# Optimization experiments

Measured on AMD Instinct MI355X. Metric: run time of the kernel, lower is better.

The kernel has to match this reference:

```python
import math
import jax, jax.numpy as jnp
from jax import lax
import numpy as np

B, DIM, H, W = 8, 256, 64, 64
D_STATE, D_CONV, EXPAND = 16, 4, 2
D_INNER = EXPAND * DIM
DT_RANK = math.ceil(DIM / 16)
POS_LEN = 16
EPS = 1e-5
GN_GROUPS = 32


def setup_inputs() -> dict:
    key = jax.random.key(0)
    ks = iter(jax.random.split(key, 24))
    rn = lambda shape, s=0.02: jax.random.normal(next(ks), shape, jnp.float32) * s
    inp = {}
    inp["x"] = jax.random.normal(next(ks), (B, DIM, H, W), jnp.float32)
    inp["pos_emb"] = rn((1, DIM, POS_LEN), 1.0)
    inp["ln_g"] = jnp.ones((DIM,), jnp.float32)
    inp["ln_b"] = jnp.zeros((DIM,), jnp.float32)
    inp["m_in_w"] = rn((2, 2 * D_INNER, DIM))
    inp["m_conv_w"] = rn((2, D_INNER, D_CONV), 0.1)
    inp["m_conv_b"] = jnp.zeros((2, D_INNER), jnp.float32)
    inp["m_xproj_w"] = rn((2, DT_RANK + 2 * D_STATE, D_INNER))
    inp["m_dt_w"] = rn((2, D_INNER, DT_RANK), 0.1)
    inp["m_dt_b"] = rn((2, D_INNER), 0.1)
    inp["m_A_log"] = jnp.tile(jnp.log(jnp.arange(1, D_STATE + 1, dtype=jnp.float32))[None, None, :], (2, D_INNER, 1))
    inp["m_D"] = jnp.ones((2, D_INNER), jnp.float32)
    inp["m_out_w"] = rn((2, DIM, D_INNER))
    inp["proj_w"] = rn((DIM, 2 * DIM))
    inp["proj_b"] = jnp.zeros((DIM,), jnp.float32)
    inp["up_dw_w"] = rn((DIM, 1, 3, 3), 0.1)
    inp["up_bn1_g"] = jnp.ones((DIM,), jnp.float32)
    inp["up_bn1_b"] = jnp.zeros((DIM,), jnp.float32)
    inp["up_pw_w"] = rn((DIM, DIM), 0.05)
    inp["up_bn2_g"] = jnp.ones((DIM,), jnp.float32)
    inp["up_bn2_b"] = jnp.zeros((DIM,), jnp.float32)
    inp["down_pw_w"] = rn((DIM, DIM), 0.05)
    inp["down_bn_g"] = jnp.ones((DIM,), jnp.float32)
    inp["down_bn_b"] = jnp.zeros((DIM,), jnp.float32)
    inp["gn_g"] = jnp.ones((DIM,), jnp.float32)
    inp["gn_b"] = jnp.zeros((DIM,), jnp.float32)
    return inp


def reference(x, pos_emb, ln_g, ln_b, m_in_w, m_conv_w, m_conv_b, m_xproj_w, m_dt_w, m_dt_b,
              m_A_log, m_D, m_out_w, proj_w, proj_b, up_dw_w, up_bn1_g, up_bn1_b, up_pw_w,
              up_bn2_g, up_bn2_b, down_pw_w, down_bn_g, down_bn_b, gn_g, gn_b):
    Bx, C, Hh, Ww = x.shape

    def ln(t):  # LayerNorm over last dim (shared self.norm)
        m = jnp.mean(t, -1, keepdims=True)
        v = jnp.mean((t - m) ** 2, -1, keepdims=True)
        return (t - m) * lax.rsqrt(v + EPS) * ln_g + ln_b

    def bn(t, g, b):  # BatchNorm2d in eval mode with default running stats (mean 0, var 1)
        return t * (g / jnp.sqrt(1.0 + EPS))[None, :, None, None] + b[None, :, None, None]

    def gn(t):  # GroupNorm(32, C), shared params (self.bn)
        Bn, Cn, Hn, Wn = t.shape
        tg = t.reshape(Bn, GN_GROUPS, Cn // GN_GROUPS, Hn, Wn)
        m = jnp.mean(tg, (2, 3, 4), keepdims=True)
        v = jnp.mean((tg - m) ** 2, (2, 3, 4), keepdims=True)
        tg = (tg - m) * lax.rsqrt(v + EPS)
        return tg.reshape(Bn, Cn, Hn, Wn) * gn_g[None, :, None, None] + gn_b[None, :, None, None]

    def interp_pos(N):  # F.interpolate(pos_embed, size=N, mode='linear', align_corners=False)
        coords = jnp.maximum((jnp.arange(N, dtype=jnp.float32) + 0.5) * (POS_LEN / N) - 0.5, 0.0)
        i0 = jnp.floor(coords).astype(jnp.int32)
        i1 = jnp.minimum(i0 + 1, POS_LEN - 1)
        wgt = coords - i0.astype(jnp.float32)
        return pos_emb[:, :, i0] * (1.0 - wgt) + pos_emb[:, :, i1] * wgt  # (1,C,N)

    def pe_branch(vals, idx, N):  # vals (B,C,N); indices interp at same size = identity
        t = vals + interp_pos(N) + idx.astype(jnp.float32)
        return ln(jnp.swapaxes(t, 1, 2))  # (B,N,C)

    def mamba(u, d):  # standard mamba_ssm selective scan; u (B,L,C)
        xz = jnp.einsum('blc,ic->bli', u, m_in_w[d])
        xh, zg = jnp.split(xz, 2, -1)
        xc = lax.conv_general_dilated(jnp.swapaxes(xh, 1, 2), m_conv_w[d][:, None, :], (1,),
                                      [(D_CONV - 1, 0)], feature_group_count=D_INNER,
                                      dimension_numbers=('NCH', 'OIH', 'NCH'))
        xc = jnp.swapaxes(jax.nn.silu(xc + m_conv_b[d][None, :, None]), 1, 2)  # (B,L,di)
        dbl = jnp.einsum('bld,ed->ble', xc, m_xproj_w[d])
        dt = dbl[..., :DT_RANK]
        Bm = dbl[..., DT_RANK:DT_RANK + D_STATE]
        Cm = dbl[..., DT_RANK + D_STATE:]
        dt = jax.nn.softplus(jnp.einsum('blr,dr->bld', dt, m_dt_w[d]) + m_dt_b[d])  # (B,L,di)
        A = -jnp.exp(m_A_log[d])  # (di,ds)
        dA = jnp.exp(dt[..., None] * A)  # (B,L,di,ds)
        dBx = dt[..., None] * Bm[:, :, None, :] * xc[..., None]

        def step(h, inps):
            dA_t, dBx_t, C_t = inps
            h = dA_t * h + dBx_t
            return h, jnp.einsum('bds,bs->bd', h, C_t)

        h0 = jnp.zeros((u.shape[0], D_INNER, D_STATE), u.dtype)
        _, ys = lax.scan(step, h0, (jnp.swapaxes(dA, 0, 1), jnp.swapaxes(dBx, 0, 1), jnp.swapaxes(Cm, 0, 1)))
        y = jnp.swapaxes(ys, 0, 1) + xc * m_D[d]
        y = y * jax.nn.silu(zg)
        return jnp.einsum('bld,od->blo', y, m_out_w[d])

    # z branch: depthwise ConvTranspose2d(k3,s2,p1,op1) + BN + ReLU + pw conv + BN, then ReLU6
    z = lax.conv_general_dilated(x, jnp.flip(up_dw_w, (2, 3)), (1, 1), [(1, 2), (1, 2)],
                                 lhs_dilation=(2, 2), feature_group_count=C,
                                 dimension_numbers=('NCHW', 'OIHW', 'NCHW'))  # (B,C,2H,2W)
    z = jax.nn.relu(bn(z, up_bn1_g, up_bn1_b))
    z = jnp.einsum('bchw,oc->bohw', z, up_pw_w)
    z = jnp.clip(bn(z, up_bn2_g, up_bn2_b), 0.0, 6.0)

    col_max = pe_branch(jnp.max(x, 2), jnp.argmax(x, 2), Ww)
    col_min = pe_branch(jnp.min(x, 2), jnp.argmin(x, 2), Ww)
    row_max = pe_branch(jnp.max(x, 3), jnp.argmax(x, 3), Hh)
    row_min = pe_branch(jnp.min(x, 3), jnp.argmin(x, 3), Hh)
    result_max = jnp.concatenate([col_max, row_max], 1)  # (B, W+H, C)
    result_min = jnp.concatenate([col_min, row_min], 1)

    fm_max = ln(mamba(result_max, 0))
    fm_min = ln(mamba(result_min, 0))
    bm_max = ln(mamba(jnp.flip(result_max, 1), 1))
    bm_min = ln(mamba(jnp.flip(result_min, 1), 1))

    res_max = jnp.concatenate([fm_max, jnp.flip(bm_max, 1)], -1) @ proj_w.T + proj_b
    res_min = jnp.concatenate([fm_min, jnp.flip(bm_min, 1)], -1) @ proj_w.T + proj_b
    res_max = ln(res_max)[:, :, None, :]  # (B,L,1,C)
    res_min = ln(res_min)[:, None, :, :]  # (B,1,L,C)

    res = jnp.transpose(res_max + res_min, (0, 3, 1, 2))  # (B,C,L,L), L=H+W=2H
    res = jnp.clip(res + 3.0, 0.0, 6.0) / 6.0 * z  # h_sigmoid gate
    res = gn(res)
    res = jnp.einsum('bchw,oc->bohw', res[:, :, ::2, ::2], down_pw_w)  # pw conv stride 2
    res = bn(res, down_bn_g, down_bn_b)
    res = gn(res)
    res = res + x
    res = gn(res)
    return res
```

## Files before the change

### kernel.cpp

```cpp
#include <hip/hip_runtime.h>
#include <hip/hip_bf16.h>
#include <math.h>

typedef __hip_bfloat16 bf16;
typedef __attribute__((ext_vector_type(8))) short short8_t;
typedef __attribute__((ext_vector_type(4))) short short4_t;
typedef __attribute__((ext_vector_type(4))) float f32x4_t;

#define EPSV 1e-5f
#define BNSC 0.99999500003749968f

__device__ __forceinline__ float bf2f(bf16 v){ return __bfloat162float(v); }
__device__ __forceinline__ bf16 f2bf(float v){ return __float2bfloat16(v); }

__device__ __forceinline__ float blk_sum(float v, float* sm){
  int tid = threadIdx.x;
  #pragma unroll
  for(int o=32;o>0;o>>=1) v += __shfl_down(v, o, 64);
  if((tid&63)==0) sm[tid>>6] = v;
  __syncthreads();
  float s = 0.f;
  int nw = blockDim.x>>6;
  for(int i=0;i<nw;i++) s += sm[i];
  __syncthreads();
  return s;
}

__device__ __forceinline__ float softplusf(float x){
  return (x > 20.f) ? x : __logf(1.f + __expf(x));
}
__device__ __forceinline__ float siluf(float x){
  return x / (1.f + __expf(-x));
}

__global__ void prep_weights(const float* __restrict__ in_w, const float* __restrict__ out_w,
                             const float* __restrict__ pw_w, const float* __restrict__ dpw_w,
                             const float* __restrict__ proj_w, const float* __restrict__ xproj_w,
                             bf16* __restrict__ Winb, bf16* __restrict__ Woutb,
                             bf16* __restrict__ Wub, bf16* __restrict__ Wdb,
                             bf16* __restrict__ Wxpb, float* __restrict__ PT,
                             float* __restrict__ gacc){
  int idx = blockIdx.x*256 + threadIdx.x;
  if(idx < 6656) gacc[idx] = 0.f;
  if(idx < 524288){ Winb[idx] = f2bf(in_w[idx]); return; }
  if(idx < 786432){ int i=idx-524288; Woutb[i] = f2bf(out_w[i]); return; }
  if(idx < 851968){ int i=idx-786432; Wub[i] = f2bf(pw_w[i]); return; }
  if(idx < 917504){ int i=idx-851968; Wdb[i] = f2bf(dpw_w[i]); return; }
  if(idx < 1048576){
    int k = idx - 917504;
    int i = k >> 9, j = k & 511;
    PT[j*256 + i] = proj_w[k];
    return;
  }
  int i = idx - 1048576;
  Wxpb[i] = f2bf(xproj_w[i]);
}

__global__ __launch_bounds__(256)
void r1_reduce_pe(const float* __restrict__ x, const float* __restrict__ pe,
                  float* __restrict__ pmax, float* __restrict__ pmin,
                  float* __restrict__ xs, float* __restrict__ xq){
  __shared__ float tile[64*65];
  __shared__ float rs_[4], rq_[4];
  int bc = blockIdx.x;
  int b = bc >> 8, c = bc & 255;
  const float* xp = x + ((size_t)bc << 12);
  float s = 0.f, q = 0.f;
  for(int i=threadIdx.x; i<4096; i+=256){
    float v = xp[i];
    tile[(i>>6)*65 + (i&63)] = v;
    s += v; q += v*v;
  }
  #pragma unroll
  for(int o=32;o>0;o>>=1){ s += __shfl_down(s, o, 64); q += __shfl_down(q, o, 64); }
  int wv = threadIdx.x >> 6, t = threadIdx.x & 63;
  if(t == 0){ rs_[wv] = s; rq_[wv] = q; }
  __syncthreads();
  if(threadIdx.x == 0){
    xs[bc] = rs_[0]+rs_[1]+rs_[2]+rs_[3];
    xq[bc] = rq_[0]+rq_[1]+rq_[2]+rq_[3];
  }
  if(wv >= 2) return;
  float coords = fmaxf((t + 0.5f)*0.25f - 0.5f, 0.f);
  int i0 = (int)floorf(coords);
  int i1 = min(i0+1, 15);
  float wg = coords - (float)i0;
  float pos = pe[c*16+i0]*(1.f-wg) + pe[c*16+i1]*wg;
  if(wv == 0){
    float cmx=-3.4e38f, cmn=3.4e38f; int cax=0, can=0;
    for(int h=0;h<64;h++){
      float v = tile[h*65 + t];
      if(v > cmx){ cmx=v; cax=h; }
      if(v < cmn){ cmn=v; can=h; }
    }
    size_t base_col = ((size_t)b*128 + t)*256 + c;
    pmax[base_col] = cmx + pos + (float)cax;
    pmin[base_col] = cmn + pos + (float)can;
  } else {
    float rmx=-3.4e38f, rmn=3.4e38f; int rax=0, ran=0;
    for(int w=0;w<64;w++){
      float v = tile[t*65 + w];
      if(v > rmx){ rmx=v; rax=w; }
      if(v < rmn){ rmn=v; ran=w; }
    }
    size_t base_row = ((size_t)b*128 + 64 + t)*256 + c;
    pmax[base_row] = rmx + pos + (float)rax;
    pmin[base_row] = rmn + pos + (float)ran;
  }
}

__global__ void ln_rows2(float* __restrict__ bufA, float* __restrict__ bufB,
                         const float* __restrict__ g, const float* __restrict__ bb,
                         bf16* __restrict__ boutA, bf16* __restrict__ boutB){
  __shared__ float sm[8];
  int row = blockIdx.x, t = threadIdx.x;
  float* buf; bf16* bout;
  if(row < 1024){ buf = bufA; bout = boutA; }
  else { buf = bufB; bout = boutB; row -= 1024; }
  float v = buf[(size_t)row*256 + t];
  float m = blk_sum(v, sm) * (1.f/256.f);
  float dv = v - m;
  float var = blk_sum(dv*dv, sm) * (1.f/256.f);
  float r = dv * rsqrtf(var + EPSV) * g[t] + bb[t];
  buf[(size_t)row*256 + t] = r;
  if(bout) bout[(size_t)row*256 + t] = f2bf(r);
}

__global__ __launch_bounds__(256,2)
void m1_mfma(const bf16* __restrict__ ubmax, const bf16* __restrict__ ubmin,
             const bf16* __restrict__ Win, float* __restrict__ xz){
  __shared__ bf16 att[64*264];
  int bx = blockIdx.x;
  int it = bx & 3, lt = (bx>>2)&1, b = (bx>>3)&7, r = bx>>6;
  int d = r & 1;
  const bf16* u = (r < 2) ? ubmax : ubmin;
  int flip = r & 1;
  int t = threadIdx.x;
  {
    int pr = t>>5, cc = (t&31)*8;
    #pragma unroll
    for(int i=0;i<8;i++){
      int p = pr + i*8;
      int l = lt*64 + p;
      int le = flip ? (127 - l) : l;
      short8_t v = *(const short8_t*)((const short*)u + ((size_t)(b*128 + le))*256 + cc);
      *(short8_t*)&att[p*264 + cc] = v;
    }
  }
  __syncthreads();
  int wv = t>>6, lane = t&63, quad = lane>>4, l16 = lane&15;
  int m0 = wv*64;
  f32x4_t acc[4][4];
  #pragma unroll
  for(int ms=0;ms<4;ms++)
    #pragma unroll
    for(int ns=0;ns<4;ns++) acc[ms][ns] = (f32x4_t){0.f,0.f,0.f,0.f};
  const short* wbase = (const short*)Win + ((size_t)d*1024 + it*256)*256;
  for(int k0=0;k0<256;k0+=32){
    short8_t afr[4], bfr[4];
    #pragma unroll
    for(int ms=0;ms<4;ms++)
      afr[ms] = *(const short8_t*)(wbase + (size_t)(m0 + ms*16 + l16)*256 + k0 + quad*8);
    #pragma unroll
    for(int ns=0;ns<4;ns++)
      bfr[ns] = *(const short8_t*)&att[(ns*16 + l16)*264 + k0 + quad*8];
    #pragma unroll
    for(int ms=0;ms<4;ms++)
      #pragma unroll
      for(int ns=0;ns<4;ns++)
        acc[ms][ns] = __builtin_amdgcn_mfma_f32_16x16x32_bf16(afr[ms], bfr[ns], acc[ms][ns], 0,0,0);
  }
  int rb = r*8 + b;
  #pragma unroll
  for(int ns=0;ns<4;ns++){
    int l = lt*64 + ns*16 + l16;
    float* dst = xz + ((size_t)rb*128 + l)*1024 + it*256;
    #pragma unroll
    for(int ms=0;ms<4;ms++){
      int i = m0 + ms*16 + quad*4;
      *(f32x4_t*)(dst + i) = acc[ms][ns];
    }
  }
}

__global__ __launch_bounds__(256)
void m2_conv(const float* __restrict__ xz, const float* __restrict__ cw,
             const float* __restrict__ cb, float* __restrict__ xc,
             bf16* __restrict__ xcb){
  int i4 = blockIdx.x*256 + threadIdx.x;
  int idx = i4 << 2;
  int row = idx >> 9, dd = idx & 511;
  int gl = row & 127;
  int d = (row >> 10) & 1;
  const float* src = xz + (size_t)row*1024 + dd;
  const float* cwp = cw + (size_t)(d*512 + dd)*4;
  f32x4_t w0 = *(const f32x4_t*)(cwp);
  f32x4_t w1 = *(const f32x4_t*)(cwp+4);
  f32x4_t w2 = *(const f32x4_t*)(cwp+8);
  f32x4_t w3 = *(const f32x4_t*)(cwp+12);
  f32x4_t bias = *(const f32x4_t*)(cb + d*512 + dd);
  f32x4_t z4 = (f32x4_t){0.f,0.f,0.f,0.f};
  f32x4_t t3 = *(const f32x4_t*)(src);
  f32x4_t t2 = (gl>=1) ? *(const f32x4_t*)(src-1024) : z4;
  f32x4_t t1 = (gl>=2) ? *(const f32x4_t*)(src-2048) : z4;
  f32x4_t t0 = (gl>=3) ? *(const f32x4_t*)(src-3072) : z4;
  f32x4_t o;
  o[0] = bias[0] + t0[0]*w0[0] + t1[0]*w0[1] + t2[0]*w0[2] + t3[0]*w0[3];
  o[1] = bias[1] + t0[1]*w1[0] + t1[1]*w1[1] + t2[1]*w1[2] + t3[1]*w1[3];
  o[2] = bias[2] + t0[2]*w2[0] + t1[2]*w2[1] + t2[2]*w2[2] + t3[2]*w2[3];
  o[3] = bias[3] + t0[3]*w3[0] + t1[3]*w3[1] + t2[3]*w3[2] + t3[3]*w3[3];
  alignas(8) bf16 ob[4];
  #pragma unroll
  for(int r=0;r<4;r++){ o[r] = siluf(o[r]); ob[r] = f2bf(o[r]); }
  *(f32x4_t*)(xc + idx) = o;
  *(short4_t*)((short*)xcb + idx) = *(const short4_t*)ob;
}

__global__ __launch_bounds__(256)
void m3_xproj(const bf16* __restrict__ xcb, const bf16* __restrict__ Wxpb,
              float* __restrict__ dbl){
  int r0 = blockIdx.x * 64;
  int d = (r0 >> 10) & 1;
  int t = threadIdx.x;
  int wv = t>>6, lane = t&63, quad = lane>>4, l16 = lane&15;
  int rowl = wv*16 + l16;
  const short* bbase = (const short*)xcb + (size_t)(r0 + rowl)*512;
  const short* abase = (const short*)Wxpb + (size_t)d*48*512;
  f32x4_t acc[3];
  #pragma unroll
  for(int ms=0;ms<3;ms++) acc[ms] = (f32x4_t){0.f,0.f,0.f,0.f};
  #pragma unroll 4
  for(int k0=0;k0<512;k0+=32){
    short8_t bfr = *(const short8_t*)(bbase + k0 + quad*8);
    short8_t afr[3];
    #pragma unroll
    for(int ms=0;ms<3;ms++)
      afr[ms] = *(const short8_t*)(abase + (size_t)(ms*16 + l16)*512 + k0 + quad*8);
    #pragma unroll
    for(int ms=0;ms<3;ms++)
      acc[ms] = __builtin_amdgcn_mfma_f32_16x16x32_bf16(afr[ms], bfr, acc[ms], 0,0,0);
  }
  float* dst = dbl + (size_t)(r0 + rowl)*48;
  #pragma unroll
  for(int ms=0;ms<3;ms++)
    *(f32x4_t*)(dst + ms*16 + quad*4) = acc[ms];
}

__global__ __launch_bounds__(256)
void m4_dt(const float* __restrict__ dbl, const float* __restrict__ dtw,
           const float* __restrict__ dtbias, float* __restrict__ dt){
  int i4 = blockIdx.x*256 + threadIdx.x;
  int idx = i4 << 2;
  int row = idx >> 9, dd = idx & 511;
  int d = (row >> 10) & 1;
  const float* dr = dbl + (size_t)row*48;
  f32x4_t dr0 = *(const f32x4_t*)(dr);
  f32x4_t dr1 = *(const f32x4_t*)(dr+4);
  f32x4_t dr2 = *(const f32x4_t*)(dr+8);
  f32x4_t dr3 = *(const f32x4_t*)(dr+12);
  f32x4_t bias = *(const f32x4_t*)(dtbias + d*512 + dd);
  f32x4_t o;
  #pragma unroll
  for(int j=0;j<4;j++){
    const float* wp = dtw + (size_t)(d*512 + dd + j)*16;
    f32x4_t w0 = *(const f32x4_t*)(wp);
    f32x4_t w1 = *(const f32x4_t*)(wp+4);
    f32x4_t w2 = *(const f32x4_t*)(wp+8);
    f32x4_t w3 = *(const f32x4_t*)(wp+12);
    float s = bias[j];
    s += dr0[0]*w0[0] + dr0[1]*w0[1] + dr0[2]*w0[2] + dr0[3]*w0[3];
    s += dr1[0]*w1[0] + dr1[1]*w1[1] + dr1[2]*w1[2] + dr1[3]*w1[3];
    s += dr2[0]*w2[0] + dr2[1]*w2[1] + dr2[2]*w2[2] + dr2[3]*w2[3];
    s += dr3[0]*w3[0] + dr3[1]*w3[1] + dr3[2]*w3[2] + dr3[3]*w3[3];
    o[j] = softplusf(s);
  }
  *(f32x4_t*)(dt + idx) = o;
}

__global__ void m5_passA(const float* __restrict__ dt, const float* __restrict__ xc,
                         const float* __restrict__ dbl, const float* __restrict__ Alog,
                         float* __restrict__ P, float* __restrict__ Hl){
  int bx = blockIdx.x;
  int seg = bx & 7, half = (bx>>3)&1, rb = bx>>4;
  int dd = half*256 + threadIdx.x;
  int d = (rb>>3)&1;
  float A[16], h[16], pr[16];
  #pragma unroll
  for(int s=0;s<16;s++){
    A[s] = -__expf(Alog[(size_t)(d*512 + dd)*16 + s]);
    h[s] = 0.f; pr[s] = 1.f;
  }
  int l0 = seg*16;
  for(int l=l0;l<l0+16;l++){
    size_t row = (size_t)rb*128 + l;
    float dtv = dt[row*512 + dd];
    float xcv = xc[row*512 + dd];
    float bx_ = dtv*xcv;
    const float* dr = dbl + row*48;
    #pragma unroll
    for(int s=0;s<16;s++){
      float dA = __expf(dtv*A[s]);
      pr[s] *= dA;
      h[s] = dA*h[s] + bx_*dr[16+s];
    }
  }
  size_t o = ((size_t)(rb*8 + seg)*512 + dd)*16;
  #pragma unroll
  for(int s=0;s<16;s+=4){
    *(f32x4_t*)(P  + o + s) = (f32x4_t){pr[s],pr[s+1],pr[s+2],pr[s+3]};
    *(f32x4_t*)(Hl + o + s) = (f32x4_t){h[s],h[s+1],h[s+2],h[s+3]};
  }
}

__global__ void m5_passB(const float* __restrict__ dt, const float* __restrict__ xc,
                         const float* __restrict__ dbl, const float* __restrict__ xz,
                         const float* __restrict__ Alog, const float* __restrict__ Dp,
                         const float* __restrict__ P, const float* __restrict__ Hl,
                         bf16* __restrict__ ybb){
  int bx = blockIdx.x;
  int seg = bx & 7, half = (bx>>3)&1, rb = bx>>4;
  int dd = half*256 + threadIdx.x;
  int d = (rb>>3)&1;
  float A[16], h[16];
  #pragma unroll
  for(int s=0;s<16;s++){
    A[s] = -__expf(Alog[(size_t)(d*512 + dd)*16 + s]);
    h[s] = 0.f;
  }
  for(int j=0;j<seg;j++){
    size_t o = ((size_t)(rb*8 + j)*512 + dd)*16;
    #pragma unroll
    for(int s=0;s<16;s+=4){
      f32x4_t pv = *(const f32x4_t*)(P + o + s);
      f32x4_t hv = *(const f32x4_t*)(Hl + o + s);
      h[s]   = pv[0]*h[s]   + hv[0];
      h[s+1] = pv[1]*h[s+1] + hv[1];
      h[s+2] = pv[2]*h[s+2] + hv[2];
      h[s+3] = pv[3]*h[s+3] + hv[3];
    }
  }
  float Dv = Dp[d*512 + dd];
  int l0 = seg*16;
  for(int l=l0;l<l0+16;l++){
    size_t row = (size_t)rb*128 + l;
    float dtv = dt[row*512 + dd];
    float xcv = xc[row*512 + dd];
    float zgv = xz[row*1024 + 512 + dd];
    const float* dr = dbl + row*48;
    float bx_ = dtv*xcv;
    float y = 0.f;
    #pragma unroll
    for(int s=0;s<16;s++){
      h[s] = __expf(dtv*A[s])*h[s] + bx_*dr[16+s];
      y += h[s]*dr[32+s];
    }
    ybb[row*512 + dd] = f2bf((y + xcv*Dv) * siluf(zgv));
  }
}

__global__ __launch_bounds__(256,2)
void m6_mfma(const bf16* __restrict__ ybb, const bf16* __restrict__ Wout,
             const float* __restrict__ lng, const float* __restrict__ lnb,
             float* __restrict__ mo){
  __shared__ char smem[64*264*4];
  bf16* ybt = (bf16*)smem;
  float* fbuf = (float*)smem;
  int bx = blockIdx.x;
  int lt = bx & 1, b = (bx>>1)&7, r = bx>>4;
  int d = r & 1, rb = r*8 + b;
  size_t rowbase = (size_t)rb*128 + lt*64;
  int t = threadIdx.x;
  for(int i=t;i<4096;i+=256){
    int row = i>>6, c8 = (i&63)*8;
    short8_t v = *(const short8_t*)((const short*)ybb + (rowbase + row)*512 + c8);
    *(short8_t*)&ybt[row*520 + c8] = v;
  }
  __syncthreads();
  int wv = t>>6, lane = t&63, quad = lane>>4, l16 = lane&15;
  int m0 = wv*64;
  f32x4_t acc[4][4];
  #pragma unroll
  for(int ms=0;ms<4;ms++)
    #pragma unroll
    for(int ns=0;ns<4;ns++) acc[ms][ns] = (f32x4_t){0.f,0.f,0.f,0.f};
  const short* wbase = (const short*)Wout + (size_t)d*256*512;
  for(int k0=0;k0<512;k0+=32){
    short8_t afr[4], bfr[4];
    #pragma unroll
    for(int ms=0;ms<4;ms++)
      afr[ms] = *(const short8_t*)(wbase + (size_t)(m0 + ms*16 + l16)*512 + k0 + quad*8);
    #pragma unroll
    for(int ns=0;ns<4;ns++)
      bfr[ns] = *(const short8_t*)&ybt[(ns*16 + l16)*520 + k0 + quad*8];
    #pragma unroll
    for(int ms=0;ms<4;ms++)
      #pragma unroll
      for(int ns=0;ns<4;ns++)
        acc[ms][ns] = __builtin_amdgcn_mfma_f32_16x16x32_bf16(afr[ms], bfr[ns], acc[ms][ns], 0,0,0);
  }
  __syncthreads();
  #pragma unroll
  for(int ns=0;ns<4;ns++){
    int row = ns*16 + l16;
    #pragma unroll
    for(int ms=0;ms<4;ms++){
      int o = m0 + ms*16 + quad*4;
      *(f32x4_t*)(fbuf + row*264 + o) = acc[ms][ns];
    }
  }
  __syncthreads();
  {
    int row = t >> 2, part = t & 3;
    const float* fr = fbuf + row*264;
    float s = 0.f;
    #pragma unroll 8
    for(int j=0;j<64;j++){
      int col = part*64 + ((j + part*16) & 63);
      s += fr[col];
    }
    s += __shfl_xor(s, 1, 64);
    s += __shfl_xor(s, 2, 64);
    float m = s * (1.f/256.f);
    float q = 0.f;
    #pragma unroll 8
    for(int j=0;j<64;j++){
      int col = part*64 + ((j + part*16) & 63);
      float dv = fr[col] - m;
      q += dv*dv;
    }
    q += __shfl_xor(q, 1, 64);
    q += __shfl_xor(q, 2, 64);
    float rs = rsqrtf(q*(1.f/256.f) + EPSV);
    float* dst = mo + (rowbase + row)*256;
    for(int j=0;j<64;j++){
      int col = part*64 + j;
      dst[col] = (fr[col] - m)*rs*lng[col] + lnb[col];
    }
  }
}

__global__ void m7_proj(const float* __restrict__ mo, const float* __restrict__ PT,
                        const float* __restrict__ pb, const float* __restrict__ lng,
                        const float* __restrict__ lnb, float* __restrict__ resm,
                        float* __restrict__ resn){
  __shared__ float ct[16*512];
  __shared__ float fbuf[16*264];
  int bx = blockIdx.x;
  int tt = bx >> 6, rem = bx & 63, b = rem >> 3, lt = rem & 7;
  int fr_ = tt*2, br = tt*2 + 1;
  for(int i=threadIdx.x;i<16*512;i+=256){
    int lr = i >> 9, k = i & 511;
    int l = lt*16 + lr;
    ct[i] = (k < 256)
      ? mo[(((size_t)(fr_*8+b)*128) + l)*256 + k]
      : mo[(((size_t)(br*8+b)*128) + (127-l))*256 + (k-256)];
  }
  __syncthreads();
  float acc[16];
  #pragma unroll
  for(int q=0;q<16;q++) acc[q] = 0.f;
  int t = threadIdx.x;
  for(int k=0;k<512;k++){
    float pv = PT[(size_t)k*256 + t];
    #pragma unroll
    for(int q=0;q<16;q++) acc[q] += pv * ct[(q<<9) + k];
  }
  float bias = pb[t];
  #pragma unroll
  for(int q=0;q<16;q++) fbuf[q*264 + t] = acc[q] + bias;
  __syncthreads();
  float* dstbuf = tt ? resn : resm;
  if(t < 64){
    int row = t >> 2, part = t & 3;
    const float* fr = fbuf + row*264;
    float s = 0.f;
    for(int j=0;j<64;j++){
      int col = part*64 + ((j + part*16) & 63);
      s += fr[col];
    }
    s += __shfl_xor(s, 1, 64);
    s += __shfl_xor(s, 2, 64);
    float m = s * (1.f/256.f);
    float q = 0.f;
    for(int j=0;j<64;j++){
      int col = part*64 + ((j + part*16) & 63);
      float dv = fr[col] - m;
      q += dv*dv;
    }
    q += __shfl_xor(q, 1, 64);
    q += __shfl_xor(q, 2, 64);
    float rs = rsqrtf(q*(1.f/256.f) + EPSV);
    float* dst = dstbuf + ((size_t)b*128 + lt*16 + row)*256;
    for(int j=0;j<64;j++){
      int col = part*64 + j;
      dst[col] = (fr[col] - m)*rs*lng[col] + lnb[col];
    }
  }
}

__global__ __launch_bounds__(256)
void k1_deconv_T(const float* __restrict__ x, const float* __restrict__ wdw,
                 const float* __restrict__ g1, const float* __restrict__ b1,
                 bf16* __restrict__ zT){
  __shared__ float in[2*64*33];
  __shared__ bf16 ot[64*80];
  int bx = blockIdx.x;
  int cb = bx & 3, half = (bx>>2)&1, h = (bx>>3)&127, b = bx>>10;
  int c0 = cb*64, w0 = half*64, iw0 = w0>>1;
  int h_odd = h & 1;
  int ihA = h_odd ? (h-1)>>1 : h>>1;
  int ihB = (h+1)>>1;
  bool hasB = h_odd && (ihB < 64);
  for(int i = threadIdx.x; i < 4224; i += 256){
    int row = i / 2112;
    int rem = i - row*2112;
    int c = rem / 33;
    int iw = rem - c*33;
    int ihl = row ? ihB : ihA;
    bool valid = (iw0 + iw < 64) && (row == 0 || hasB);
    in[i] = valid ? x[(((size_t)b*256 + c0 + c)<<12) + (ihl<<6) + iw0 + iw] : 0.f;
  }
  __syncthreads();
  int c = threadIdx.x & 63, g = threadIdx.x >> 6;
  const float* wp = wdw + (c0+c)*9;
  int khA3 = h_odd ? 6 : 3;
  float wA0 = wp[khA3], wA1 = wp[khA3+1], wA2 = wp[khA3+2];
  float wB0 = wp[0],    wB1 = wp[1],      wB2 = wp[2];
  float scale = g1[c0+c]*BNSC, bias = b1[c0+c];
  const float* inA = in + c*33;
  const float* inB = in + 2112 + c*33;
  #pragma unroll
  for(int i=0;i<16;i++){
    int wi = g*16 + i;
    float s;
    if(!(i&1)){
      int iw = wi>>1;
      s = inA[iw]*wA1 + inB[iw]*wB1;
    } else {
      int iwa = (wi-1)>>1, iwb = (wi+1)>>1;
      s = inA[iwa]*wA2 + inA[iwb]*wA0 + inB[iwa]*wB2 + inB[iwb]*wB0;
    }
    ot[wi*80 + c] = f2bf(fmaxf(s*scale + bias, 0.f));
  }
  __syncthreads();
  int rr = threadIdx.x >> 3;
  int co = (threadIdx.x & 7) * 8;
  size_t obase = (((size_t)b*16384) + (size_t)h*128 + w0)*256 + c0;
  #pragma unroll
  for(int pass=0; pass<2; pass++){
    int wi = rr + pass*32;
    short8_t v = *(const short8_t*)&ot[wi*80 + co];
    *(short8_t*)((short*)zT + obase + (size_t)wi*256 + co) = v;
  }
}

__global__ __launch_bounds__(256,2)
void k2_mfma(const bf16* __restrict__ zT, const bf16* __restrict__ Wub,
             const float* __restrict__ g2, const float* __restrict__ b2,
             const float* __restrict__ resm, const float* __restrict__ resn,
             bf16* __restrict__ resS, float* __restrict__ gsum1, float* __restrict__ gssq1){
  __shared__ bf16 zt[128*264];
  __shared__ float rm_s[256];
  __shared__ float gn_s[32], gn_q[32];
  int b = blockIdx.y;
  int p0 = blockIdx.x*128;
  int h = p0 >> 7;
  int t = threadIdx.x;
  if(t < 32){ gn_s[t] = 0.f; gn_q[t] = 0.f; }
  if(t >= 64 && t < 128){
    int tt = t - 64;
    *(f32x4_t*)&rm_s[tt*4] = *(const f32x4_t*)(resm + ((size_t)b*128 + h)*256 + tt*4);
  }
  {
    const short* src = (const short*)zT + (((size_t)b*16384 + p0)*256);
    int pr = t>>5;
    int cc = (t&31)*8;
    #pragma unroll
    for(int i=0;i<16;i++){
      int p = pr + i*8;
      short8_t v = *(const short8_t*)(src + (size_t)p*256 + cc);
      *(short8_t*)&zt[p*264 + cc] = v;
    }
  }
  __syncthreads();
  int wv = t>>6, lane = t&63, quad = lane>>4, l16 = lane&15;
  int m0 = wv*64;
  f32x4_t acc[4][8];
  #pragma unroll
  for(int ms=0;ms<4;ms++)
    #pragma unroll
    for(int ns=0;ns<8;ns++) acc[ms][ns] = (f32x4_t){0.f,0.f,0.f,0.f};
  const short* wp = (const short*)Wub + (size_t)(m0 + l16)*256 + quad*8;
  short8_t afr[4];
  #pragma unroll
  for(int ms=0;ms<4;ms++) afr[ms] = *(const short8_t*)(wp + (size_t)ms*16*256);
  for(int k0=0;k0<256;k0+=32){
    short8_t anext[4];
    if(k0 + 32 < 256){
      #pragma unroll
      for(int ms=0;ms<4;ms++)
        anext[ms] = *(const short8_t*)(wp + (size_t)ms*16*256 + k0 + 32);
    }
    short8_t bfr[8];
    #pragma unroll
    for(int ns=0;ns<8;ns++)
      bfr[ns] = *(const short8_t*)&zt[(ns*16 + l16)*264 + k0 + quad*8];
    #pragma unroll
    for(int ms=0;ms<4;ms++)
      #pragma unroll
      for(int ns=0;ns<8;ns++)
        acc[ms][ns] = __builtin_amdgcn_mfma_f32_16x16x32_bf16(afr[ms], bfr[ns], acc[ms][ns], 0,0,0);
    #pragma unroll
    for(int ms=0;ms<4;ms++) afr[ms] = anext[ms];
  }
  __syncthreads();
  bool h_even = ((h & 1) == 0);
  float sg[4], qg[4];
  #pragma unroll
  for(int ms=0;ms<4;ms++){ sg[ms]=0.f; qg[ms]=0.f; }
  #pragma unroll
  for(int ns=0;ns<8;ns++){
    int pl = ns*16 + l16;
    const float* rn = resn + ((size_t)b*128 + pl)*256;
    bool store = h_even && ((pl & 1) == 0);
    #pragma unroll
    for(int ms=0;ms<4;ms++){
      int o = m0 + ms*16 + quad*4;
      f32x4_t a = acc[ms][ns];
      f32x4_t gv = *(const f32x4_t*)(g2+o);
      f32x4_t bv = *(const f32x4_t*)(b2+o);
      f32x4_t rmv = *(const f32x4_t*)&rm_s[o];
      f32x4_t rnv = *(const f32x4_t*)(rn+o);
      alignas(8) bf16 ov[4];
      #pragma unroll
      for(int r=0;r<4;r++){
        float zv = a[r]*(gv[r]*BNSC) + bv[r];
        zv = fminf(fmaxf(zv, 0.f), 6.f);
        float gate = fminf(fmaxf(rmv[r]+rnv[r]+3.f, 0.f), 6.f)*(1.f/6.f);
        float vo = zv*gate;
        ov[r] = f2bf(vo);
        sg[ms] += vo;
        qg[ms] += vo*vo;
      }
      if(store) *(short4_t*)&zt[pl*264 + o] = *(const short4_t*)ov;
    }
  }
  #pragma unroll
  for(int ms=0;ms<4;ms++){
    float S = sg[ms], Q = qg[ms];
    S += __shfl_xor(S, 1, 64);  Q += __shfl_xor(Q, 1, 64);
    S += __shfl_xor(S, 2, 64);  Q += __shfl_xor(Q, 2, 64);
    S += __shfl_xor(S, 4, 64);  Q += __shfl_xor(Q, 4, 64);
    S += __shfl_xor(S, 8, 64);  Q += __shfl_xor(Q, 8, 64);
    if(l16 == 0){
      int o = m0 + ms*16 + quad*4;
      atomicAdd(&gn_s[o>>3], S);
      atomicAdd(&gn_q[o>>3], Q);
    }
  }
  __syncthreads();
  if(t < 32){
    atomicAdd(&gsum1[b*32 + t], gn_s[t]);
    atomicAdd(&gssq1[b*32 + t], gn_q[t]);
  }
  if(h_even){
    short* dst = (short*)resS + ((size_t)b*4096 + (h>>1)*64)*256;
    #pragma unroll
    for(int it=0; it<8; it++){
      int slot = t + it*256;
      int row = slot >> 5;
      int co = (slot & 31)*8;
      short8_t v = *(const short8_t*)&zt[(row*2)*264 + co];
      *(short8_t*)(dst + (size_t)row*256 + co) = v;
    }
  }
}

__global__ __launch_bounds__(256,2)
void k4_mfma(const bf16* __restrict__ resS, const bf16* __restrict__ Wdb,
             const float* __restrict__ gsum1, const float* __restrict__ gssq1,
             const float* __restrict__ gng, const float* __restrict__ gnb,
             const float* __restrict__ dbg, const float* __restrict__ dbb,
             const float* __restrict__ x, float* __restrict__ t1,
             float* __restrict__ t1s, float* __restrict__ t1q, float* __restrict__ t1x){
  __shared__ bf16 at[128*264];
  __shared__ float sc[256], sb[256];
  __shared__ float stm[32], str[32];
  int b = blockIdx.y;
  int q0 = blockIdx.x*128;
  int t = threadIdx.x;
  if(t < 32){
    float m = gsum1[b*32+t] * (1.f/131072.f);
    float var = gssq1[b*32+t] * (1.f/131072.f) - m*m;
    stm[t] = m;
    str[t] = rsqrtf(var + EPSV);
  }
  __syncthreads();
  {
    int cch = t, g = cch>>3;
    float m = stm[g], rs = str[g];
    float s = rs*gng[cch];
    sc[cch] = s; sb[cch] = gnb[cch] - m*s;
  }
  __syncthreads();
  {
    int pr = t>>5;
    int cc = (t&31)*8;
    const short* src = (const short*)resS + ((size_t)b*4096 + q0)*256;
    #pragma unroll
    for(int i=0;i<16;i++){
      int q = pr + i*8;
      short8_t v = *(const short8_t*)(src + (size_t)q*256 + cc);
      const bf16* vv = (const bf16*)&v;
      alignas(16) bf16 ov[8];
      #pragma unroll
      for(int j=0;j<8;j++) ov[j] = f2bf(bf2f(vv[j])*sc[cc+j] + sb[cc+j]);
      *(short8_t*)&at[q*264 + cc] = *(const short8_t*)ov;
    }
  }
  __syncthreads();
  int wv = t>>6, lane = t&63, quad = lane>>4, l16 = lane&15;
  int n0 = wv*64;
  f32x4_t acc[8][4];
  #pragma unroll
  for(int ms=0;ms<8;ms++)
    #pragma unroll
    for(int ns=0;ns<4;ns++) acc[ms][ns] = (f32x4_t){0.f,0.f,0.f,0.f};
  const short* wp = (const short*)Wdb + (size_t)(n0 + l16)*256 + quad*8;
  short8_t bfr[4];
  #pragma unroll
  for(int ns=0;ns<4;ns++) bfr[ns] = *(const short8_t*)(wp + (size_t)ns*16*256);
  for(int k0=0;k0<256;k0+=32){
    short8_t bnext[4];
    if(k0 + 32 < 256){
      #pragma unroll
      for(int ns=0;ns<4;ns++)
        bnext[ns] = *(const short8_t*)(wp + (size_t)ns*16*256 + k0 + 32);
    }
    short8_t afr[8];
    #pragma unroll
    for(int ms=0;ms<8;ms++)
      afr[ms] = *(const short8_t*)&at[(ms*16 + l16)*264 + k0 + quad*8];
    #pragma unroll
    for(int ms=0;ms<8;ms++)
      #pragma unroll
      for(int ns=0;ns<4;ns++)
        acc[ms][ns] = __builtin_amdgcn_mfma_f32_16x16x32_bf16(afr[ms], bfr[ns], acc[ms][ns], 0,0,0);
    #pragma unroll
    for(int ns=0;ns<4;ns++) bfr[ns] = bnext[ns];
  }
  #pragma unroll
  for(int ns=0;ns<4;ns++){
    int o = n0 + ns*16 + l16;
    float s2 = dbg[o]*BNSC, bb2 = dbb[o];
    float* dst = t1 + (((size_t)b*256 + o) << 12);
    const float* xsrc = x + (((size_t)b*256 + o) << 12);
    float s_=0.f, q_=0.f, c_=0.f;
    #pragma unroll
    for(int ms=0;ms<8;ms++){
      int ps = q0 + ms*16 + quad*4;
      f32x4_t a = acc[ms][ns];
      f32x4_t xv = *(const f32x4_t*)(xsrc + ps);
      f32x4_t ov;
      #pragma unroll
      for(int r=0;r<4;r++){
        ov[r] = a[r]*s2 + bb2;
        s_ += ov[r];
        q_ += ov[r]*ov[r];
        c_ += ov[r]*xv[r];
      }
      *(f32x4_t*)(dst + ps) = ov;
    }
    s_ += __shfl_xor(s_, 16, 64);
    q_ += __shfl_xor(q_, 16, 64);
    c_ += __shfl_xor(c_, 16, 64);
    s_ += __shfl_xor(s_, 32, 64);
    q_ += __shfl_xor(q_, 32, 64);
    c_ += __shfl_xor(c_, 32, 64);
    if(quad == 0){
      atomicAdd(&t1s[b*256 + o], s_);
      atomicAdd(&t1q[b*256 + o], q_);
      atomicAdd(&t1x[b*256 + o], c_);
    }
  }
}

__global__ void compose_gn(const float* __restrict__ t1s, const float* __restrict__ t1q,
                           const float* __restrict__ t1x, const float* __restrict__ xs,
                           const float* __restrict__ xq, const float* __restrict__ gng,
                           const float* __restrict__ gnb,
                           float* __restrict__ cA, float* __restrict__ cB, float* __restrict__ cC){
  int b = blockIdx.x, c = threadIdx.x;
  int i = b*256 + c;
  float ts = t1s[i], tq = t1q[i], tx = t1x[i];
  float sx = xs[i], qx = xq[i];
  float gs = ts, gq = tq;
  gs += __shfl_xor(gs,1,64); gq += __shfl_xor(gq,1,64);
  gs += __shfl_xor(gs,2,64); gq += __shfl_xor(gq,2,64);
  gs += __shfl_xor(gs,4,64); gq += __shfl_xor(gq,4,64);
  float m2 = gs*(1.f/32768.f);
  float v2 = gq*(1.f/32768.f) - m2*m2;
  float rs2 = rsqrtf(v2 + EPSV);
  float a  = rs2*gng[c];
  float bb = gnb[c] - m2*a;
  float Su = a*ts + 4096.f*bb + sx;
  float Qu = a*a*tq + 4096.f*bb*bb + qx + 2.f*a*bb*ts + 2.f*a*tx + 2.f*bb*sx;
  float gSu = Su, gQu = Qu;
  gSu += __shfl_xor(gSu,1,64); gQu += __shfl_xor(gQu,1,64);
  gSu += __shfl_xor(gSu,2,64); gQu += __shfl_xor(gQu,2,64);
  gSu += __shfl_xor(gSu,4,64); gQu += __shfl_xor(gQu,4,64);
  float m3 = gSu*(1.f/32768.f);
  float v3 = gQu*(1.f/32768.f) - m3*m3;
  float rs3 = rsqrtf(v3 + EPSV);
  float s3 = rs3*gng[c];
  cA[i] = a*s3;
  cB[i] = s3;
  cC[i] = (bb - m3)*s3 + gnb[c];
}

__global__ void k8_gn_out(const float* __restrict__ t1, const float* __restrict__ x,
                          const float* __restrict__ cA, const float* __restrict__ cB,
                          const float* __restrict__ cC, float* __restrict__ out){
  int i4 = blockIdx.x*256 + threadIdx.x;
  int idx = i4 << 2;
  int c = (idx >> 12) & 255, b = idx >> 20;
  int i = b*256 + c;
  float A = cA[i], Bv = cB[i], C = cC[i];
  f32x4_t tv = *(const f32x4_t*)(t1 + idx);
  f32x4_t xv = *(const f32x4_t*)(x + idx);
  f32x4_t ov;
  #pragma unroll
  for(int r=0;r<4;r++) ov[r] = A*tv[r] + Bv*xv[r] + C;
  *(f32x4_t*)(out + idx) = ov;
}

extern "C" void kernel_launch(void* const* d_in, const int* in_sizes, int n_in,
                              void* d_out, int out_size, void* d_ws, size_t ws_size,
                              hipStream_t stream){
  const float* x      = (const float*)d_in[0];
  const float* pos    = (const float*)d_in[1];
  const float* ln_g   = (const float*)d_in[2];
  const float* ln_b   = (const float*)d_in[3];
  const float* in_w   = (const float*)d_in[4];
  const float* conv_w = (const float*)d_in[5];
  const float* conv_b = (const float*)d_in[6];
  const float* xproj  = (const float*)d_in[7];
  const float* dt_w   = (const float*)d_in[8];
  const float* dt_b   = (const float*)d_in[9];
  const float* A_log  = (const float*)d_in[10];
  const float* Dp     = (const float*)d_in[11];
  const float* out_w  = (const float*)d_in[12];
  const float* proj_w = (const float*)d_in[13];
  const float* proj_b = (const float*)d_in[14];
  const float* dw_w   = (const float*)d_in[15];
  const float* bn1g   = (const float*)d_in[16];
  const float* bn1b   = (const float*)d_in[17];
  const float* pw_w   = (const float*)d_in[18];
  const float* bn2g   = (const float*)d_in[19];
  const float* bn2b   = (const float*)d_in[20];
  const float* dpw_w  = (const float*)d_in[21];
  const float* dbng   = (const float*)d_in[22];
  const float* dbnb   = (const float*)d_in[23];
  const float* gng    = (const float*)d_in[24];
  const float* gnb    = (const float*)d_in[25];
  float* out = (float*)d_out;

  float* ws = (float*)d_ws;
  bf16*  resS = (bf16*)ws;
  bf16*  zT   = (bf16*)(ws + 16777216);
  float* scanP = ws + 16777216;
  float* scanH = ws + 16777216 + 2097152;
  float* zone = ws + 33554432;
  float* xz   = zone;
  float* xc   = xz  + 4194304;
  float* dbl  = xc  + 2097152;
  float* dtb  = dbl + 196608;
  bf16*  ybb  = (bf16*)(dtb + 2097152);
  bf16*  xcb  = (bf16*)(dtb + 2097152 + 524288);
  float* t1   = zone;
  float* mo   = zone + 9633792;
  float* resm = mo   + 1048576;
  float* resn = resm + 262144;
  float* pmax = resn + 262144;
  float* pmin = pmax + 262144;
  float* PT   = pmin + 262144;
  bf16*  ubmax= (bf16*)(PT + 131072);
  bf16*  ubmin= (bf16*)(PT + 131072 + 131072);
  bf16*  Winb = (bf16*)(PT + 131072 + 262144);
  bf16*  Woutb= (bf16*)(PT + 131072 + 524288);
  bf16*  Wub  = (bf16*)(PT + 131072 + 655360);
  bf16*  Wdb  = (bf16*)(PT + 131072 + 688128);
  bf16*  Wxpb = (bf16*)(PT + 131072 + 720896);
  float* gacc = PT + 131072 + 745472;
  float* gsum1 = gacc,        *gssq1 = gacc + 256;
  float* t1s = gacc + 512;
  float* t1q = gacc + 2560;
  float* t1x = gacc + 4608;
  float* xs  = gacc + 6656;
  float* xq  = gacc + 8704;
  float* cA  = gacc + 10752;
  float* cB  = gacc + 12800;
  float* cC  = gacc + 14848;

  prep_weights<<<4288,256,0,stream>>>(in_w, out_w, pw_w, dpw_w, proj_w, xproj,
                                      Winb, Woutb, Wub, Wdb, Wxpb, PT, gacc);

  r1_reduce_pe<<<2048,256,0,stream>>>(x, pos, pmax, pmin, xs, xq);
  ln_rows2<<<2048,256,0,stream>>>(pmax, pmin, ln_g, ln_b, ubmax, ubmin);

  m1_mfma<<<256,256,0,stream>>>(ubmax, ubmin, Winb, xz);
  m2_conv<<<2048,256,0,stream>>>(xz, conv_w, conv_b, xc, xcb);
  m3_xproj<<<64,256,0,stream>>>(xcb, Wxpb, dbl);
  m4_dt<<<2048,256,0,stream>>>(dbl, dt_w, dt_b, dtb);
  m5_passA<<<512,256,0,stream>>>(dtb, xc, dbl, A_log, scanP, scanH);
  m5_passB<<<512,256,0,stream>>>(dtb, xc, dbl, xz, A_log, Dp, scanP, scanH, ybb);
  m6_mfma<<<64,256,0,stream>>>(ybb, Woutb, ln_g, ln_b, mo);
  m7_proj<<<128,256,0,stream>>>(mo, PT, proj_b, ln_g, ln_b, resm, resn);

  k1_deconv_T<<<8192,256,0,stream>>>(x, dw_w, bn1g, bn1b, zT);
  k2_mfma<<<dim3(128,8),256,0,stream>>>(zT, Wub, bn2g, bn2b, resm, resn, resS,
                                        gsum1, gssq1);

  k4_mfma<<<dim3(32,8),256,0,stream>>>(resS, Wdb, gsum1, gssq1,
                                       gng, gnb, dbng, dbnb, x, t1, t1s, t1q, t1x);

  compose_gn<<<8,256,0,stream>>>(t1s, t1q, t1x, xs, xq, gng, gnb, cA, cB, cC);
  k8_gn_out<<<8192,256,0,stream>>>(t1, x, cA, cB, cC, out);
}
```

Baseline: 464.4 us.

## Halve k4 tile for occupancy, fuse compose_gn into output kernel, shrink k2 staging

Three independent changes. k4_mfma now processes 64 positions per block instead of 128, with half the accumulators and LDS, launch bounds raised to 4 blocks per SM, and twice as many blocks. The tiny compose_gn kernel is removed and every thread of k8_gn_out recomputes the group-norm coefficients from the per-channel sums, saving a launch at the cost of redundant scalar work per thread. k2's shared staging buffer now stores only even rows, compacting the LDS index.

```diff
diff --git a/kernel.cpp b/kernel.cpp
--- a/kernel.cpp
+++ b/kernel.cpp
@@ -642,7 +642,7 @@
         sg[ms] += vo;
         qg[ms] += vo*vo;
       }
-      if(store) *(short4_t*)&zt[pl*264 + o] = *(const short4_t*)ov;
+      if(store) *(short4_t*)&zt[(pl>>1)*264 + o] = *(const short4_t*)ov;
     }
   }
   #pragma unroll
@@ -670,24 +670,24 @@
       int slot = t + it*256;
       int row = slot >> 5;
       int co = (slot & 31)*8;
-      short8_t v = *(const short8_t*)&zt[(row*2)*264 + co];
+      short8_t v = *(const short8_t*)&zt[(row)*264 + co];
       *(short8_t*)(dst + (size_t)row*256 + co) = v;
     }
   }
 }
 
-__global__ __launch_bounds__(256,2)
+__global__ __launch_bounds__(256,4)
 void k4_mfma(const bf16* __restrict__ resS, const bf16* __restrict__ Wdb,
              const float* __restrict__ gsum1, const float* __restrict__ gssq1,
              const float* __restrict__ gng, const float* __restrict__ gnb,
              const float* __restrict__ dbg, const float* __restrict__ dbb,
              const float* __restrict__ x, float* __restrict__ t1,
              float* __restrict__ t1s, float* __restrict__ t1q, float* __restrict__ t1x){
-  __shared__ bf16 at[128*264];
+  __shared__ bf16 at[64*264];
   __shared__ float sc[256], sb[256];
   __shared__ float stm[32], str[32];
   int b = blockIdx.y;
-  int q0 = blockIdx.x*128;
+  int q0 = blockIdx.x*64;
   int t = threadIdx.x;
   if(t < 32){
     float m = gsum1[b*32+t] * (1.f/131072.f);
@@ -708,7 +708,7 @@
     int cc = (t&31)*8;
     const short* src = (const short*)resS + ((size_t)b*4096 + q0)*256;
     #pragma unroll
-    for(int i=0;i<16;i++){
+    for(int i=0;i<8;i++){
       int q = pr + i*8;
       short8_t v = *(const short8_t*)(src + (size_t)q*256 + cc);
       const bf16* vv = (const bf16*)&v;
@@ -721,9 +721,9 @@
   __syncthreads();
   int wv = t>>6, lane = t&63, quad = lane>>4, l16 = lane&15;
   int n0 = wv*64;
-  f32x4_t acc[8][4];
-  #pragma unroll
-  for(int ms=0;ms<8;ms++)
+  f32x4_t acc[4][4];
+  #pragma unroll
+  for(int ms=0;ms<4;ms++)
     #pragma unroll
     for(int ns=0;ns<4;ns++) acc[ms][ns] = (f32x4_t){0.f,0.f,0.f,0.f};
   const short* wp = (const short*)Wdb + (size_t)(n0 + l16)*256 + quad*8;
@@ -737,12 +737,12 @@
       for(int ns=0;ns<4;ns++)
         bnext[ns] = *(const short8_t*)(wp + (size_t)ns*16*256 + k0 + 32);
     }
-    short8_t afr[8];
-    #pragma unroll
-    for(int ms=0;ms<8;ms++)
+    short8_t afr[4];
+    #pragma unroll
+    for(int ms=0;ms<4;ms++)
       afr[ms] = *(const short8_t*)&at[(ms*16 + l16)*264 + k0 + quad*8];
     #pragma unroll
-    for(int ms=0;ms<8;ms++)
+    for(int ms=0;ms<4;ms++)
       #pragma unroll
       for(int ns=0;ns<4;ns++)
         acc[ms][ns] = __builtin_amdgcn_mfma_f32_16x16x32_bf16(afr[ms], bfr[ns], acc[ms][ns], 0,0,0);
@@ -757,7 +757,7 @@
     const float* xsrc = x + (((size_t)b*256 + o) << 12);
     float s_=0.f, q_=0.f, c_=0.f;
     #pragma unroll
-    for(int ms=0;ms<8;ms++){
+    for(int ms=0;ms<4;ms++){
       int ps = q0 + ms*16 + quad*4;
       f32x4_t a = acc[ms][ns];
       f32x4_t xv = *(const f32x4_t*)(xsrc + ps);
@@ -785,47 +785,39 @@
   }
 }
 
-__global__ void compose_gn(const float* __restrict__ t1s, const float* __restrict__ t1q,
-                           const float* __restrict__ t1x, const float* __restrict__ xs,
-                           const float* __restrict__ xq, const float* __restrict__ gng,
-                           const float* __restrict__ gnb,
-                           float* __restrict__ cA, float* __restrict__ cB, float* __restrict__ cC){
-  int b = blockIdx.x, c = threadIdx.x;
-  int i = b*256 + c;
-  float ts = t1s[i], tq = t1q[i], tx = t1x[i];
-  float sx = xs[i], qx = xq[i];
-  float gs = ts, gq = tq;
-  gs += __shfl_xor(gs,1,64); gq += __shfl_xor(gq,1,64);
-  gs += __shfl_xor(gs,2,64); gq += __shfl_xor(gq,2,64);
-  gs += __shfl_xor(gs,4,64); gq += __shfl_xor(gq,4,64);
+__global__ void k8_gn_out(const float* __restrict__ t1, const float* __restrict__ x,
+                          const float* __restrict__ t1s, const float* __restrict__ t1q,
+                          const float* __restrict__ t1x, const float* __restrict__ xs,
+                          const float* __restrict__ xq, const float* __restrict__ gng,
+                          const float* __restrict__ gnb, float* __restrict__ out){
+  int i4 = blockIdx.x*256 + threadIdx.x;
+  int idx = i4 << 2;
+  int c = (idx >> 12) & 255, b = idx >> 20;
+  int base = b*256 + (c & ~7);
+  int cb0 = c & ~7;
+  float gs = 0.f, gq = 0.f;
+  #pragma unroll
+  for(int j=0;j<8;j++){ gs += t1s[base+j]; gq += t1q[base+j]; }
   float m2 = gs*(1.f/32768.f);
   float v2 = gq*(1.f/32768.f) - m2*m2;
   float rs2 = rsqrtf(v2 + EPSV);
-  float a  = rs2*gng[c];
-  float bb = gnb[c] - m2*a;
-  float Su = a*ts + 4096.f*bb + sx;
-  float Qu = a*a*tq + 4096.f*bb*bb + qx + 2.f*a*bb*ts + 2.f*a*tx + 2.f*bb*sx;
-  float gSu = Su, gQu = Qu;
-  gSu += __shfl_xor(gSu,1,64); gQu += __shfl_xor(gQu,1,64);
-  gSu += __shfl_xor(gSu,2,64); gQu += __shfl_xor(gQu,2,64);
-  gSu += __shfl_xor(gSu,4,64); gQu += __shfl_xor(gQu,4,64);
+  float gSu = 0.f, gQu = 0.f;
+  #pragma unroll
+  for(int j=0;j<8;j++){
+    float ts = t1s[base+j], tq = t1q[base+j], tx = t1x[base+j];
+    float sx = xs[base+j],  qx = xq[base+j];
+    float a  = rs2*gng[cb0+j];
+    float bb = gnb[cb0+j] - m2*a;
+    gSu += a*ts + 4096.f*bb + sx;
+    gQu += a*a*tq + 4096.f*bb*bb + qx + 2.f*a*bb*ts + 2.f*a*tx + 2.f*bb*sx;
+  }
   float m3 = gSu*(1.f/32768.f);
   float v3 = gQu*(1.f/32768.f) - m3*m3;
   float rs3 = rsqrtf(v3 + EPSV);
   float s3 = rs3*gng[c];
-  cA[i] = a*s3;
-  cB[i] = s3;
-  cC[i] = (bb - m3)*s3 + gnb[c];
-}
-
-__global__ void k8_gn_out(const float* __restrict__ t1, const float* __restrict__ x,
-                          const float* __restrict__ cA, const float* __restrict__ cB,
-                          const float* __restrict__ cC, float* __restrict__ out){
-  int i4 = blockIdx.x*256 + threadIdx.x;
-  int idx = i4 << 2;
-  int c = (idx >> 12) & 255, b = idx >> 20;
-  int i = b*256 + c;
-  float A = cA[i], Bv = cB[i], C = cC[i];
+  float a_c  = rs2*gng[c];
+  float bb_c = gnb[c] - m2*a_c;
+  float A = a_c*s3, Bv = s3, C = (bb_c - m3)*s3 + gnb[c];
   f32x4_t tv = *(const f32x4_t*)(t1 + idx);
   f32x4_t xv = *(const f32x4_t*)(x + idx);
   f32x4_t ov;
@@ -898,9 +890,6 @@
   float* t1x = gacc + 4608;
   float* xs  = gacc + 6656;
   float* xq  = gacc + 8704;
-  float* cA  = gacc + 10752;
-  float* cB  = gacc + 12800;
-  float* cC  = gacc + 14848;
 
   prep_weights<<<4288,256,0,stream>>>(in_w, out_w, pw_w, dpw_w, proj_w, xproj,
                                       Winb, Woutb, Wub, Wdb, Wxpb, PT, gacc);
@@ -921,9 +910,8 @@
   k2_mfma<<<dim3(128,8),256,0,stream>>>(zT, Wub, bn2g, bn2b, resm, resn, resS,
                                         gsum1, gssq1);
 
-  k4_mfma<<<dim3(32,8),256,0,stream>>>(resS, Wdb, gsum1, gssq1,
+  k4_mfma<<<dim3(64,8),256,0,stream>>>(resS, Wdb, gsum1, gssq1,
                                        gng, gnb, dbng, dbnb, x, t1, t1s, t1q, t1x);
 
-  compose_gn<<<8,256,0,stream>>>(t1s, t1q, t1x, xs, xq, gng, gnb, cA, cB, cC);
-  k8_gn_out<<<8192,256,0,stream>>>(t1, x, cA, cB, cC, out);
-}
+  k8_gn_out<<<8192,256,0,stream>>>(t1, x, t1s, t1q, t1x, xs, xq, gng, gnb, out);
+}
```

New measurement: 463.0 us. No clear change (-0.3%).
